# Kernel tuning notes

Hardware: AMD Instinct MI355X
Metric: run time of the kernel (lower is better)

## Reference

```python
import jax, jax.numpy as jnp
import numpy as np

N, E, C, H = 100000, 3200000, 4, 64
EPS = 1e-8


def setup_inputs() -> dict:
    key = jax.random.key(0)
    k1, k2, k3, k4, k5, k6, k7 = jax.random.split(key, 7)
    x = jax.random.uniform(k1, (N, C), dtype=jnp.float32)            # [pm10, u10, v10, aux]
    pos = jax.random.normal(k2, (N, 2), dtype=jnp.float32)           # node coordinates
    edge_index = jax.random.randint(k3, (2, E), 0, N, dtype=jnp.int64)
    # PhysicsFluxLayer edge MLP: in = [x_i, x_j, wind_proj, dist] -> hidden
    fan_in = 2 * C + 2
    mlp_w = jax.random.normal(k4, (H, fan_in), dtype=jnp.float32) / np.sqrt(fan_in)
    mlp_b = jnp.zeros((H,), dtype=jnp.float32)
    # output head (module inits to zero; use small random values for a non-degenerate baseline)
    head_w = jax.random.normal(k5, (1, H), dtype=jnp.float32) * 0.02
    head_b = jax.random.normal(k6, (1,), dtype=jnp.float32) * 0.02
    return {"x": x, "pos": pos, "mlp_w": mlp_w, "mlp_b": mlp_b,
            "head_w": head_w, "head_b": head_b, "edge_index": edge_index}


def reference(x, pos, mlp_w, mlp_b, head_w, head_b, edge_index):
    src = edge_index[0]   # j (message source)
    dst = edge_index[1]   # i (message target)
    u10, v10 = x[:, 1], x[:, 2]
    # edge geometry: direction i -> j and distance
    d = pos[src] - pos[dst]                                  # [E,2]
    dist = jnp.sqrt(jnp.sum(d * d, axis=1) + EPS)            # [E]
    dhat = d / dist[:, None]
    # source wind projected onto the edge direction (advective transport term)
    wind_proj = u10[src] * dhat[:, 0] + v10[src] * dhat[:, 1]  # [E]
    edge_feat = jnp.concatenate(
        [x[dst], x[src], wind_proj[:, None], dist[:, None]], axis=1)  # [E, 2C+2]
    msg = jax.nn.relu(edge_feat @ mlp_w.T + mlp_b)            # [E,H]
    flux = jax.ops.segment_sum(msg, dst, num_segments=N)      # [N,H] scatter-add
    delta_pm10 = flux @ head_w.T + head_b                     # [N,1]
    pm10_next = jax.nn.softplus(x[:, 0:1] + delta_pm10)       # [N,1]
    return pm10_next, delta_pm10
```

## Files before the change

### kernel.cpp

```cpp
#include <hip/hip_runtime.h>
#include <hip/hip_bf16.h>


#define HID    64
#define EPSV   1e-8f
#define BNODES 256
#define CAP    10240
#define MAXB   512
#define BLK_SC 512
#define RPT_SC 25
#define LSTAGE (BLK_SC * RPT_SC)
#define BLK_C  256
#define SLOTW  20
#define OVF_CAP 65536

typedef _Float16 half8 __attribute__((ext_vector_type(8)));
typedef _Float16 half2_t __attribute__((ext_vector_type(2)));
typedef float f32x4 __attribute__((ext_vector_type(4)));

__device__ __forceinline__ unsigned int packh2(float a, float b) {
    union { half2_t h; unsigned int u; } v;
    v.h = half2_t{(_Float16)a, (_Float16)b};
    return v.u;
}

__device__ __forceinline__ void feat_from_rows(float4 xs, float4 ps4,
                                               float4 xd, float4 pd4,
                                               float* f) {
    float d0 = ps4.x - pd4.x;
    float d1 = ps4.y - pd4.y;
    float dist = sqrtf(fmaf(d0, d0, fmaf(d1, d1, EPSV)));
    float inv = 1.0f / dist;
    float wind = (xs.y * d0 + xs.z * d1) * inv;
    f[0] = xd.x; f[1] = xd.y; f[2] = xd.z; f[3] = xd.w;
    f[4] = xs.x; f[5] = xs.y; f[6] = xs.z; f[7] = xs.w;
    f[8] = wind; f[9] = dist;
}

__device__ __forceinline__ float mlp_scalar_g(const float* __restrict__ mlp_w,
                                              const float* __restrict__ mlp_b,
                                              const float* __restrict__ head_w,
                                              const float* f) {
    float sacc = 0.0f;
    for (int h = 0; h < HID; h++) {
        const float* wr = mlp_w + h * 10;
        float a = mlp_b[h];
        a = fmaf(wr[0], f[0], a); a = fmaf(wr[1], f[1], a);
        a = fmaf(wr[2], f[2], a); a = fmaf(wr[3], f[3], a);
        a = fmaf(wr[4], f[4], a); a = fmaf(wr[5], f[5], a);
        a = fmaf(wr[6], f[6], a); a = fmaf(wr[7], f[7], a);
        a = fmaf(wr[8], f[8], a); a = fmaf(wr[9], f[9], a);
        a = fmaxf(a, 0.0f);
        sacc = fmaf(head_w[h], a, sacc);
    }
    return sacc;
}

__global__ __launch_bounds__(512) void prep_kernel(
    const float4* __restrict__ x, const float2* __restrict__ pos,
    float4* __restrict__ xpos, float* __restrict__ delta_extra,
    unsigned long long* g_ptr64, int* ovf_cnt, int N, int PB)
{
    int n = blockIdx.x * 512 + threadIdx.x;
    if (n < N) {
        float4 xr = x[n];
        float2 pr = pos[n];
        xpos[2 * n]     = xr;
        xpos[2 * n + 1] = make_float4(pr.x, pr.y, 0.0f, 0.0f);
        delta_extra[n] = 0.0f;
    }
    if (n < PB) g_ptr64[n] = 0ull;
    if (n == 0) *ovf_cnt = 0;
}

__global__ __launch_bounds__(BLK_SC) void scatter_kernel(
    const int* __restrict__ srcs, const int* __restrict__ dsts,
    int E, int B,
    unsigned long long* g_ptr64, unsigned int* __restrict__ sorted,
    int2* __restrict__ ovf, int* ovf_cnt)
{
    __shared__ int hist[MAXB];
    __shared__ int base[MAXB];
    __shared__ int run[MAXB];
    __shared__ int wsum[BLK_SC / 64];
    __shared__ unsigned int lstage[LSTAGE];

    int tid  = threadIdx.x;
    int lane = tid & 63;
    int wid  = tid >> 6;
    int lo = blockIdx.x * (BLK_SC * RPT_SC);

    int es[RPT_SC], ed[RPT_SC];
    bool ev[RPT_SC];
    #pragma unroll
    for (int r = 0; r < RPT_SC; r++) {
        int e = lo + r * BLK_SC + tid;
        bool okr = (e < E);
        ev[r] = okr;
        int ee = okr ? e : 0;
        es[r] = srcs[ee];
        ed[r] = dsts[ee];
    }

    for (int b2 = tid; b2 < MAXB; b2 += BLK_SC) { hist[b2] = 0; run[b2] = 0; }
    __syncthreads();
    #pragma unroll
    for (int r = 0; r < RPT_SC; r++)
        if (ev[r]) atomicAdd(&hist[ed[r] >> 8], 1);
    __syncthreads();

    int PB = (B + 1) >> 1;
    for (int p = tid; p < PB; p += BLK_SC) {
        int b0 = 2 * p, b1 = 2 * p + 1;
        unsigned long long h0 = (unsigned int)hist[b0];
        unsigned long long h1 = (b1 < B) ? (unsigned int)hist[b1] : 0ull;
        unsigned long long comb = h0 | (h1 << 32);
        unsigned long long old = 0ull;
        if (comb) old = atomicAdd(&g_ptr64[p], comb);
        base[b0] = (int)(old & 0xffffffffull);
        if (b1 < B) base[b1] = (int)(old >> 32);
    }
    int v = hist[tid];
    int x = v;
    #pragma unroll
    for (int m = 1; m < 64; m <<= 1) {
        int y = __shfl_up(x, m, 64);
        if (lane >= m) x += y;
    }
    if (lane == 63) wsum[wid] = x;
    __syncthreads();
    if (tid == 0) {
        int a = 0;
        #pragma unroll
        for (int j = 0; j < BLK_SC / 64; j++) { int t = wsum[j]; wsum[j] = a; a += t; }
    }
    __syncthreads();
    hist[tid] = wsum[wid] + x - v;
    __syncthreads();

    #pragma unroll
    for (int r = 0; r < RPT_SC; r++) {
        if (ev[r]) {
            int d = ed[r];
            int b = d >> 8;
            int rk = atomicAdd(&run[b], 1);
            lstage[hist[b] + rk] =
                ((unsigned int)es[r] << 8) | (unsigned int)(d & 255);
        }
    }
    __syncthreads();

    for (int b = wid; b < B; b += BLK_SC / 64) {
        int cnt = run[b];
        int gb  = base[b];
        int lp  = hist[b];
        for (int t = lane; t < cnt; t += 64) {
            unsigned int pay = lstage[lp + t];
            int rel = gb + t;
            if (rel < CAP) {
                sorted[(size_t)b * CAP + rel] = pay;
            } else {
                int o = atomicAdd(ovf_cnt, 1);
                if (o < OVF_CAP)
                    ovf[o] = make_int2((int)(pay >> 8), (b << 8) | (int)(pay & 255u));
            }
        }
    }
}

__global__ __launch_bounds__(BLK_C, 4) void compute_kernel(
    const float4* __restrict__ xpos,
    const float* __restrict__ mlp_w, const float* __restrict__ mlp_b,
    const float* __restrict__ head_w,
    const unsigned int* __restrict__ sorted,
    const unsigned long long* __restrict__ g_ptr64,
    float* __restrict__ partial, int BB, int ksh)
{
    __shared__ __align__(16) unsigned int stage[4 * 64 * SLOTW];
    __shared__ float acc[BNODES];
    int tid  = threadIdx.x;
    int wave = tid >> 6;
    int lane = tid & 63;
    int col  = lane & 15;
    int quad = lane >> 4;
    int wbase = wave * 64 * SLOTW;

    acc[tid] = 0.0f;

    {
        unsigned int* slotp = &stage[wbase + lane * SLOTW];
        slotp[5] = 0u;
        *(uint2*)(slotp + 6) = make_uint2(0u, 0u);
        *(uint4*)(slotp + 8) = make_uint4(0u, 0u, 0u, 0u);
        *(uint4*)(slotp + 12) = make_uint4(0u, 0u, 0u, 0u);
    }

    half8 wfr[4];
    f32x4 bias4[4], hw4[4];
    #pragma unroll
    for (int c = 0; c < 4; c++) {
        int h = c * 16 + col;
        half8 wf = half8{0, 0, 0, 0, 0, 0, 0, 0};
        if (quad == 0) {
            #pragma unroll
            for (int j = 0; j < 8; j++) wf[j] = (_Float16)mlp_w[h * 10 + j];
        } else if (quad == 1) {
            wf[0] = (_Float16)mlp_w[h * 10 + 8];
            wf[1] = (_Float16)mlp_w[h * 10 + 9];
        }
        wfr[c] = wf;
        bias4[c] = *(const f32x4*)&mlp_b[c * 16 + quad * 4];
        hw4[c]   = *(const f32x4*)&head_w[c * 16 + quad * 4];
    }
    __syncthreads();

    int b    = blockIdx.x >> ksh;
    int part = blockIdx.x & ((1 << ksh) - 1);
    unsigned long long gp = g_ptr64[b >> 1];
    int cnt = (b & 1) ? (int)(gp >> 32) : (int)(gp & 0xffffffffull);
    cnt = min(cnt, CAP);
    int e0 = (cnt * part) >> ksh;
    int e1 = (cnt * (part + 1)) >> ksh;
    const unsigned int* sp = sorted + (size_t)b * CAP;
    int nbase = b << 8;

    int i = e0 + tid;
    bool ok = (i < e1);
    unsigned int pay = (e0 < e1) ? sp[ok ? i : e0] : 0u;
    int s  = (int)(pay >> 8);
    int dl = (int)(pay & 255u);
    float4 xs  = xpos[2 * s];
    float4 ps4 = xpos[2 * s + 1];
    float4 xd  = xpos[2 * (nbase + dl)];
    float4 pd4 = xpos[2 * (nbase + dl) + 1];

    for (int i0 = e0; i0 < e1; i0 += BLK_C) {
        bool cok = ok;
        int  cdl = dl;
        float f[10];
        feat_from_rows(xs, ps4, xd, pd4, f);
        unsigned int pk0 = packh2(f[0], f[1]);
        unsigned int pk1 = packh2(f[2], f[3]);
        unsigned int pk2 = packh2(f[4], f[5]);
        unsigned int pk3 = packh2(f[6], f[7]);
        unsigned int pk4 = packh2(f[8], f[9]);

        int ni = i0 + BLK_C + tid;
        ok = (ni < e1);
        pay = sp[ok ? ni : e0];
        s  = (int)(pay >> 8);
        dl = (int)(pay & 255u);
        xs  = xpos[2 * s];
        ps4 = xpos[2 * s + 1];
        xd  = xpos[2 * (nbase + dl)];
        pd4 = xpos[2 * (nbase + dl) + 1];

        unsigned int* slotp = &stage[wbase + lane * SLOTW];
        *(uint4*)slotp = make_uint4(pk0, pk1, pk2, pk3);
        slotp[4] = pk4;

        float mysum = 0.0f;
        #pragma unroll
        for (int eg = 0; eg < 4; eg++) {
            const half8 fb = *(const half8*)&stage[wbase + (eg * 16 + col) * SLOTW + quad * 4];
            float sacc = 0.0f;
            #pragma unroll
            for (int c = 0; c < 4; c++) {
                f32x4 d = __builtin_amdgcn_mfma_f32_16x16x32_f16(wfr[c], fb, bias4[c], 0, 0, 0);
                sacc = fmaf(hw4[c][0], fmaxf(d[0], 0.f), sacc);
                sacc = fmaf(hw4[c][1], fmaxf(d[1], 0.f), sacc);
                sacc = fmaf(hw4[c][2], fmaxf(d[2], 0.f), sacc);
                sacc = fmaf(hw4[c][3], fmaxf(d[3], 0.f), sacc);
            }
            sacc += __shfl_xor(sacc, 16, 64);
            sacc += __shfl_xor(sacc, 32, 64);
            if (quad == eg) mysum = sacc;
        }
        if (cok) atomicAdd(&acc[cdl], mysum);
    }
    __syncthreads();
    partial[(size_t)part * BB + nbase + tid] = acc[tid];
}

__global__ __launch_bounds__(256) void ovf_kernel(
    const float4* __restrict__ x, const float2* __restrict__ pos,
    const float* __restrict__ mlp_w, const float* __restrict__ mlp_b,
    const float* __restrict__ head_w,
    const int2* __restrict__ ovf, const int* __restrict__ ovf_cnt,
    float* __restrict__ delta_extra)
{
    int cnt = min(*ovf_cnt, OVF_CAP);
    for (int i = blockIdx.x * blockDim.x + threadIdx.x; i < cnt;
         i += gridDim.x * blockDim.x) {
        int2 sd = ovf[i];
        float4 xs = x[sd.x], xd = x[sd.y];
        float2 ps = pos[sd.x], pd = pos[sd.y];
        float f[10];
        feat_from_rows(xs, make_float4(ps.x, ps.y, 0, 0),
                       xd, make_float4(pd.x, pd.y, 0, 0), f);
        unsafeAtomicAdd(&delta_extra[sd.y], mlp_scalar_g(mlp_w, mlp_b, head_w, f));
    }
}

__global__ __launch_bounds__(512) void final_kernel(
    const float* __restrict__ xf,
    const float* __restrict__ partial, int BB,
    const float* __restrict__ delta_extra,
    const float* __restrict__ head_b,
    float* __restrict__ out, int N, int kpart)
{
    int n = blockIdx.x * 512 + threadIdx.x;
    if (n >= N) return;
    float delta = delta_extra[n] + head_b[0];
    for (int p = 0; p < kpart; p++)
        delta += partial[(size_t)p * BB + n];
    float v = xf[4 * n] + delta;
    float sp = fmaxf(v, 0.0f) + log1pf(expf(-fabsf(v)));
    out[n] = sp;
    out[N + n] = delta;
}

__global__ __launch_bounds__(256) void edge_kernel_fallback(
    const float4* __restrict__ x, const float2* __restrict__ pos,
    const float* __restrict__ mlp_w, const float* __restrict__ mlp_b,
    const float* __restrict__ head_w,
    const int* __restrict__ srcs, const int* __restrict__ dsts,
    float* __restrict__ delta_acc, int E)
{
    long e = (long)blockIdx.x * 256 + threadIdx.x;
    if (e >= E) return;
    int s = srcs[e], d = dsts[e];
    float4 xs = x[s], xd = x[d];
    float2 ps = pos[s], pd = pos[d];
    float f[10];
    feat_from_rows(xs, make_float4(ps.x, ps.y, 0, 0),
                   xd, make_float4(pd.x, pd.y, 0, 0), f);
    unsafeAtomicAdd(&delta_acc[d], mlp_scalar_g(mlp_w, mlp_b, head_w, f));
}

__global__ __launch_bounds__(256) void node_kernel_fallback(
    const float* __restrict__ xf, const float* __restrict__ delta_acc,
    const float* __restrict__ head_b, float* __restrict__ out, int N)
{
    int n = blockIdx.x * 256 + threadIdx.x;
    if (n >= N) return;
    float delta = delta_acc[n] + head_b[0];
    float v = xf[4 * n] + delta;
    float sp = fmaxf(v, 0.0f) + log1pf(expf(-fabsf(v)));
    out[n] = sp;
    out[N + n] = delta;
}

static inline size_t align_up(size_t v, size_t a) { return (v + a - 1) & ~(a - 1); }

extern "C" void kernel_launch(void* const* d_in, const int* in_sizes, int n_in,
                              void* d_out, int out_size, void* d_ws, size_t ws_size,
                              hipStream_t stream) {
    const float4* x      = (const float4*)d_in[0];
    const float2* pos    = (const float2*)d_in[1];
    const float*  mlp_w  = (const float*)d_in[2];
    const float*  mlp_b  = (const float*)d_in[3];
    const float*  head_w = (const float*)d_in[4];
    const float*  head_b = (const float*)d_in[5];
    const int*    ei     = (const int*)d_in[6];

    int N = in_sizes[0] / 4;
    int E = in_sizes[6] / 2;
    const int* srcs = ei;
    const int* dsts = ei + E;
    int B  = (N + BNODES - 1) / BNODES;
    int PB = (B + 1) >> 1;
    int BB = B * BNODES;

    size_t off = 0;
    float* delta_extra = (float*)((char*)d_ws + off);
    off = align_up(off + (size_t)N * 4, 256);
    float4* xpos = (float4*)((char*)d_ws + off);
    off = align_up(off + (size_t)N * 32, 256);
    unsigned long long* g_ptr64 = (unsigned long long*)((char*)d_ws + off);
    off = align_up(off + (size_t)PB * 8, 256);
    int* ovf_cnt = (int*)((char*)d_ws + off);
    off = align_up(off + 64, 256);
    int2* ovf = (int2*)((char*)d_ws + off);
    off = align_up(off + (size_t)OVF_CAP * 8, 256);
    unsigned int* sorted = (unsigned int*)((char*)d_ws + off);
    off = align_up(off + (size_t)B * CAP * 4, 256);
    float* partial = (float*)((char*)d_ws + off);

    int kpart = 8, ksh = 3;
    if (off + (size_t)8 * BB * 4 > ws_size) { kpart = 4; ksh = 2; }
    size_t off_end = off + (size_t)kpart * BB * 4;
    bool fast = (off_end <= ws_size) && (B <= MAXB);

    if (fast) {
        int pgrid = (N + 511) / 512;
        prep_kernel<<<pgrid, 512, 0, stream>>>(x, pos, xpos, delta_extra,
                                               g_ptr64, ovf_cnt, N, PB);
        int sgrid = (E + LSTAGE - 1) / LSTAGE;
        scatter_kernel<<<sgrid, BLK_SC, 0, stream>>>(srcs, dsts, E, B,
                                                     g_ptr64, sorted, ovf, ovf_cnt);
        compute_kernel<<<B << ksh, BLK_C, 0, stream>>>(xpos, mlp_w, mlp_b, head_w,
                                                       sorted, g_ptr64, partial, BB, ksh);
        ovf_kernel<<<16, 256, 0, stream>>>(x, pos, mlp_w, mlp_b, head_w,
                                           ovf, ovf_cnt, delta_extra);
        final_kernel<<<(N + 511) / 512, 512, 0, stream>>>(
            (const float*)x, partial, BB, delta_extra, head_b, (float*)d_out, N, kpart);
    } else {
        float* delta = (float*)d_ws;
        hipMemsetAsync(delta, 0, (size_t)N * sizeof(float), stream);
        edge_kernel_fallback<<<(int)((E + 255) / 256), 256, 0, stream>>>(
            x, pos, mlp_w, mlp_b, head_w, srcs, dsts, delta, E);
        node_kernel_fallback<<<(N + 255) / 256, 256, 0, stream>>>(
            (const float*)x, delta, head_b, (float*)d_out, N);
    }
}
```

Before: 157.1 us.

## Fuse prep and overflow kernels, cache dst rows in LDS, deepen prefetch

The prep kernel is replaced by a memset plus node-row packing and fp16 weight-fragment building inside the scatter kernel. The overflow kernel is folded into the compute kernel's part-0 blocks. The scatter now ranks edges once with a single atomic pass and writes through a precomputed destination table instead of a second local atomic pass. The compute kernel stages its 256 destination rows in LDS, loads prebuilt weight fragments, and uses a three-stage software prefetch rotation. The goal is fewer launches and less gather and atomic work, at the cost of more LDS in the scatter kernel (two 12800-entry arrays), which may lower its occupancy.

```diff
diff --git a/kernel.cpp b/kernel.cpp
--- a/kernel.cpp
+++ b/kernel.cpp
@@ -56,39 +56,26 @@
     return sacc;
 }
 
-__global__ __launch_bounds__(512) void prep_kernel(
-    const float4* __restrict__ x, const float2* __restrict__ pos,
-    float4* __restrict__ xpos, float* __restrict__ delta_extra,
-    unsigned long long* g_ptr64, int* ovf_cnt, int N, int PB)
-{
-    int n = blockIdx.x * 512 + threadIdx.x;
-    if (n < N) {
-        float4 xr = x[n];
-        float2 pr = pos[n];
-        xpos[2 * n]     = xr;
-        xpos[2 * n + 1] = make_float4(pr.x, pr.y, 0.0f, 0.0f);
-        delta_extra[n] = 0.0f;
-    }
-    if (n < PB) g_ptr64[n] = 0ull;
-    if (n == 0) *ovf_cnt = 0;
-}
-
 __global__ __launch_bounds__(BLK_SC) void scatter_kernel(
     const int* __restrict__ srcs, const int* __restrict__ dsts,
-    int E, int B,
+    int E, int B, int N,
+    const float4* __restrict__ x, const float2* __restrict__ pos,
+    const float* __restrict__ mlp_w,
+    float4* __restrict__ xpos, uint4* __restrict__ wbuf,
     unsigned long long* g_ptr64, unsigned int* __restrict__ sorted,
     int2* __restrict__ ovf, int* ovf_cnt)
 {
     __shared__ int hist[MAXB];
     __shared__ int base[MAXB];
-    __shared__ int run[MAXB];
+    __shared__ int pfx[MAXB];
     __shared__ int wsum[BLK_SC / 64];
-    __shared__ unsigned int lstage[LSTAGE];
+    __shared__ unsigned int lpay[LSTAGE];
+    __shared__ unsigned int ldst[LSTAGE];
 
     int tid  = threadIdx.x;
     int lane = tid & 63;
     int wid  = tid >> 6;
-    int lo = blockIdx.x * (BLK_SC * RPT_SC);
+    int lo = blockIdx.x * LSTAGE;
 
     int es[RPT_SC], ed[RPT_SC];
     bool ev[RPT_SC];
@@ -102,11 +89,48 @@
         ed[r] = dsts[ee];
     }
 
-    for (int b2 = tid; b2 < MAXB; b2 += BLK_SC) { hist[b2] = 0; run[b2] = 0; }
-    __syncthreads();
+    for (int b2 = tid; b2 < MAXB; b2 += BLK_SC) hist[b2] = 0;
+
+    {
+        int nper = (N + gridDim.x - 1) / gridDim.x;
+        int n0 = blockIdx.x * nper;
+        int n1 = min(n0 + nper, N);
+        for (int n = n0 + tid; n < n1; n += BLK_SC) {
+            float4 xr = x[n];
+            float2 pr = pos[n];
+            xpos[2 * n]     = xr;
+            xpos[2 * n + 1] = make_float4(pr.x, pr.y, 0.0f, 0.0f);
+        }
+    }
+    if (blockIdx.x == 0 && tid < 64) {
+        int colw = tid & 15, quadw = tid >> 4;
+        #pragma unroll
+        for (int c = 0; c < 4; c++) {
+            int h = c * 16 + colw;
+            half8 wf = half8{0, 0, 0, 0, 0, 0, 0, 0};
+            if (quadw == 0) {
+                #pragma unroll
+                for (int j = 0; j < 8; j++) wf[j] = (_Float16)mlp_w[h * 10 + j];
+            } else if (quadw == 1) {
+                wf[0] = (_Float16)mlp_w[h * 10 + 8];
+                wf[1] = (_Float16)mlp_w[h * 10 + 9];
+            }
+            union { half8 h8; uint4 u4; } cv;
+            cv.h8 = wf;
+            wbuf[c * 64 + tid] = cv.u4;
+        }
+    }
+    __syncthreads();
+
     #pragma unroll
-    for (int r = 0; r < RPT_SC; r++)
-        if (ev[r]) atomicAdd(&hist[ed[r] >> 8], 1);
+    for (int r = 0; r < RPT_SC; r++) {
+        if (ev[r]) {
+            int b = ed[r] >> 8;
+            int rk = atomicAdd(&hist[b], 1);
+            es[r] = (es[r] << 8) | (ed[r] & 255);
+            ed[r] = (b << 14) | rk;
+        }
+    }
     __syncthreads();
 
     int PB = (B + 1) >> 1;
@@ -121,13 +145,13 @@
         if (b1 < B) base[b1] = (int)(old >> 32);
     }
     int v = hist[tid];
-    int x = v;
+    int xs_ = v;
     #pragma unroll
     for (int m = 1; m < 64; m <<= 1) {
-        int y = __shfl_up(x, m, 64);
-        if (lane >= m) x += y;
-    }
-    if (lane == 63) wsum[wid] = x;
+        int y = __shfl_up(xs_, m, 64);
+        if (lane >= m) xs_ += y;
+    }
+    if (lane == 63) wsum[wid] = xs_;
     __syncthreads();
     if (tid == 0) {
         int a = 0;
@@ -135,48 +159,49 @@
         for (int j = 0; j < BLK_SC / 64; j++) { int t = wsum[j]; wsum[j] = a; a += t; }
     }
     __syncthreads();
-    hist[tid] = wsum[wid] + x - v;
+    pfx[tid] = wsum[wid] + xs_ - v;
     __syncthreads();
 
     #pragma unroll
     for (int r = 0; r < RPT_SC; r++) {
         if (ev[r]) {
-            int d = ed[r];
-            int b = d >> 8;
-            int rk = atomicAdd(&run[b], 1);
-            lstage[hist[b] + rk] =
-                ((unsigned int)es[r] << 8) | (unsigned int)(d & 255);
-        }
-    }
-    __syncthreads();
-
-    for (int b = wid; b < B; b += BLK_SC / 64) {
-        int cnt = run[b];
-        int gb  = base[b];
-        int lp  = hist[b];
-        for (int t = lane; t < cnt; t += 64) {
-            unsigned int pay = lstage[lp + t];
-            int rel = gb + t;
+            int b  = ed[r] >> 14;
+            int rk = ed[r] & 0x3FFF;
+            int p  = pfx[b] + rk;
+            unsigned int pay = (unsigned int)es[r];
+            lpay[p] = pay;
+            int rel = base[b] + rk;
             if (rel < CAP) {
-                sorted[(size_t)b * CAP + rel] = pay;
+                ldst[p] = (unsigned int)b * CAP + (unsigned int)rel;
             } else {
+                ldst[p] = 0xFFFFFFFFu;
                 int o = atomicAdd(ovf_cnt, 1);
                 if (o < OVF_CAP)
                     ovf[o] = make_int2((int)(pay >> 8), (b << 8) | (int)(pay & 255u));
             }
         }
     }
+    __syncthreads();
+
+    int cnt_blk = min(E - lo, LSTAGE);
+    for (int t = tid; t < cnt_blk; t += BLK_SC) {
+        unsigned int d = ldst[t];
+        if (d != 0xFFFFFFFFu) sorted[d] = lpay[t];
+    }
 }
 
 __global__ __launch_bounds__(BLK_C, 4) void compute_kernel(
     const float4* __restrict__ xpos,
+    const uint4* __restrict__ wbuf,
     const float* __restrict__ mlp_w, const float* __restrict__ mlp_b,
     const float* __restrict__ head_w,
     const unsigned int* __restrict__ sorted,
     const unsigned long long* __restrict__ g_ptr64,
-    float* __restrict__ partial, int BB, int ksh)
+    const int2* __restrict__ ovf, const int* __restrict__ ovf_cnt,
+    float* __restrict__ partial, int BB, int ksh, int N)
 {
     __shared__ __align__(16) unsigned int stage[4 * 64 * SLOTW];
+    __shared__ __align__(16) float4 drows[2 * BNODES];
     __shared__ float acc[BNODES];
     int tid  = threadIdx.x;
     int wave = tid >> 6;
@@ -185,7 +210,17 @@
     int quad = lane >> 4;
     int wbase = wave * 64 * SLOTW;
 
+    int b    = blockIdx.x >> ksh;
+    int part = blockIdx.x & ((1 << ksh) - 1);
+    int nbase = b << 8;
+
     acc[tid] = 0.0f;
+
+    {
+        int lim = 2 * N - 1;
+        drows[tid]       = xpos[min(2 * nbase + tid, lim)];
+        drows[tid + 256] = xpos[min(2 * nbase + tid + 256, lim)];
+    }
 
     {
         unsigned int* slotp = &stage[wbase + lane * SLOTW];
@@ -199,119 +234,110 @@
     f32x4 bias4[4], hw4[4];
     #pragma unroll
     for (int c = 0; c < 4; c++) {
-        int h = c * 16 + col;
-        half8 wf = half8{0, 0, 0, 0, 0, 0, 0, 0};
-        if (quad == 0) {
-            #pragma unroll
-            for (int j = 0; j < 8; j++) wf[j] = (_Float16)mlp_w[h * 10 + j];
-        } else if (quad == 1) {
-            wf[0] = (_Float16)mlp_w[h * 10 + 8];
-            wf[1] = (_Float16)mlp_w[h * 10 + 9];
-        }
-        wfr[c] = wf;
+        union { uint4 u4; half8 h8; } cv;
+        cv.u4 = wbuf[c * 64 + lane];
+        wfr[c] = cv.h8;
         bias4[c] = *(const f32x4*)&mlp_b[c * 16 + quad * 4];
         hw4[c]   = *(const f32x4*)&head_w[c * 16 + quad * 4];
     }
     __syncthreads();
 
-    int b    = blockIdx.x >> ksh;
-    int part = blockIdx.x & ((1 << ksh) - 1);
     unsigned long long gp = g_ptr64[b >> 1];
     int cnt = (b & 1) ? (int)(gp >> 32) : (int)(gp & 0xffffffffull);
     cnt = min(cnt, CAP);
     int e0 = (cnt * part) >> ksh;
     int e1 = (cnt * (part + 1)) >> ksh;
     const unsigned int* sp = sorted + (size_t)b * CAP;
-    int nbase = b << 8;
-
-    int i = e0 + tid;
-    bool ok = (i < e1);
-    unsigned int pay = (e0 < e1) ? sp[ok ? i : e0] : 0u;
-    int s  = (int)(pay >> 8);
-    int dl = (int)(pay & 255u);
-    float4 xs  = xpos[2 * s];
-    float4 ps4 = xpos[2 * s + 1];
-    float4 xd  = xpos[2 * (nbase + dl)];
-    float4 pd4 = xpos[2 * (nbase + dl) + 1];
-
-    for (int i0 = e0; i0 < e1; i0 += BLK_C) {
-        bool cok = ok;
-        int  cdl = dl;
-        float f[10];
-        feat_from_rows(xs, ps4, xd, pd4, f);
-        unsigned int pk0 = packh2(f[0], f[1]);
-        unsigned int pk1 = packh2(f[2], f[3]);
-        unsigned int pk2 = packh2(f[4], f[5]);
-        unsigned int pk3 = packh2(f[6], f[7]);
-        unsigned int pk4 = packh2(f[8], f[9]);
-
-        int ni = i0 + BLK_C + tid;
-        ok = (ni < e1);
-        pay = sp[ok ? ni : e0];
-        s  = (int)(pay >> 8);
-        dl = (int)(pay & 255u);
-        xs  = xpos[2 * s];
-        ps4 = xpos[2 * s + 1];
-        xd  = xpos[2 * (nbase + dl)];
-        pd4 = xpos[2 * (nbase + dl) + 1];
-
-        unsigned int* slotp = &stage[wbase + lane * SLOTW];
-        *(uint4*)slotp = make_uint4(pk0, pk1, pk2, pk3);
-        slotp[4] = pk4;
-
-        float mysum = 0.0f;
-        #pragma unroll
-        for (int eg = 0; eg < 4; eg++) {
-            const half8 fb = *(const half8*)&stage[wbase + (eg * 16 + col) * SLOTW + quad * 4];
-            float sacc = 0.0f;
+
+    if (e0 < e1) {
+        unsigned int p0, p1, p2;
+        float4 xA, pA, xB, pB, xC, pC;
+        {
+            int i = e0 + tid;
+            p0 = sp[(i < e1) ? i : e0];
+            int i1 = i + BLK_C;
+            p1 = sp[(i1 < e1) ? i1 : e0];
+            int s0 = (int)(p0 >> 8);
+            xA = xpos[2 * s0];
+            pA = xpos[2 * s0 + 1];
+        }
+
+        auto body = [&](int i0, unsigned int pc, unsigned int pn,
+                        unsigned int& pn2, float4 xc, float4 psc,
+                        float4& xn, float4& psn) {
+            bool cok = (i0 + tid) < e1;
+            int dl = (int)(pc & 255u);
+            int i2 = i0 + 2 * BLK_C + tid;
+            pn2 = sp[(i2 < e1) ? i2 : e0];
+            int sn = (int)(pn >> 8);
+            xn  = xpos[2 * sn];
+            psn = xpos[2 * sn + 1];
+            float4 xd  = drows[2 * dl];
+            float4 pd4 = drows[2 * dl + 1];
+            float f[10];
+            feat_from_rows(xc, psc, xd, pd4, f);
+            unsigned int* slotp = &stage[wbase + lane * SLOTW];
+            *(uint4*)slotp = make_uint4(packh2(f[0], f[1]), packh2(f[2], f[3]),
+                                        packh2(f[4], f[5]), packh2(f[6], f[7]));
+            slotp[4] = packh2(f[8], f[9]);
+
+            float mysum = 0.0f;
             #pragma unroll
-            for (int c = 0; c < 4; c++) {
-                f32x4 d = __builtin_amdgcn_mfma_f32_16x16x32_f16(wfr[c], fb, bias4[c], 0, 0, 0);
-                sacc = fmaf(hw4[c][0], fmaxf(d[0], 0.f), sacc);
-                sacc = fmaf(hw4[c][1], fmaxf(d[1], 0.f), sacc);
-                sacc = fmaf(hw4[c][2], fmaxf(d[2], 0.f), sacc);
-                sacc = fmaf(hw4[c][3], fmaxf(d[3], 0.f), sacc);
+            for (int eg = 0; eg < 4; eg++) {
+                const half8 fb = *(const half8*)&stage[wbase + (eg * 16 + col) * SLOTW + quad * 4];
+                float sacc = 0.0f;
+                #pragma unroll
+                for (int c = 0; c < 4; c++) {
+                    f32x4 d = __builtin_amdgcn_mfma_f32_16x16x32_f16(wfr[c], fb, bias4[c], 0, 0, 0);
+                    sacc = fmaf(hw4[c][0], fmaxf(d[0], 0.f), sacc);
+                    sacc = fmaf(hw4[c][1], fmaxf(d[1], 0.f), sacc);
+                    sacc = fmaf(hw4[c][2], fmaxf(d[2], 0.f), sacc);
+                    sacc = fmaf(hw4[c][3], fmaxf(d[3], 0.f), sacc);
+                }
+                sacc += __shfl_xor(sacc, 16, 64);
+                sacc += __shfl_xor(sacc, 32, 64);
+                if (quad == eg) mysum = sacc;
             }
-            sacc += __shfl_xor(sacc, 16, 64);
-            sacc += __shfl_xor(sacc, 32, 64);
-            if (quad == eg) mysum = sacc;
-        }
-        if (cok) atomicAdd(&acc[cdl], mysum);
+            if (cok) atomicAdd(&acc[dl], mysum);
+        };
+
+        int i0 = e0;
+        for (;;) {
+            body(i0, p0, p1, p2, xA, pA, xB, pB);
+            i0 += BLK_C; if (i0 >= e1) break;
+            body(i0, p1, p2, p0, xB, pB, xC, pC);
+            i0 += BLK_C; if (i0 >= e1) break;
+            body(i0, p2, p0, p1, xC, pC, xA, pA);
+            i0 += BLK_C; if (i0 >= e1) break;
+        }
     }
     __syncthreads();
     partial[(size_t)part * BB + nbase + tid] = acc[tid];
-}
-
-__global__ __launch_bounds__(256) void ovf_kernel(
-    const float4* __restrict__ x, const float2* __restrict__ pos,
-    const float* __restrict__ mlp_w, const float* __restrict__ mlp_b,
-    const float* __restrict__ head_w,
-    const int2* __restrict__ ovf, const int* __restrict__ ovf_cnt,
-    float* __restrict__ delta_extra)
-{
-    int cnt = min(*ovf_cnt, OVF_CAP);
-    for (int i = blockIdx.x * blockDim.x + threadIdx.x; i < cnt;
-         i += gridDim.x * blockDim.x) {
-        int2 sd = ovf[i];
-        float4 xs = x[sd.x], xd = x[sd.y];
-        float2 ps = pos[sd.x], pd = pos[sd.y];
-        float f[10];
-        feat_from_rows(xs, make_float4(ps.x, ps.y, 0, 0),
-                       xd, make_float4(pd.x, pd.y, 0, 0), f);
-        unsafeAtomicAdd(&delta_extra[sd.y], mlp_scalar_g(mlp_w, mlp_b, head_w, f));
+
+    if (part == 0) {
+        __syncthreads();
+        int oc = min(*ovf_cnt, OVF_CAP);
+        for (int idx = tid; idx < oc; idx += BLK_C) {
+            int2 sd = ovf[idx];
+            if ((sd.y >> 8) == b) {
+                float f[10];
+                feat_from_rows(xpos[2 * sd.x], xpos[2 * sd.x + 1],
+                               xpos[2 * sd.y], xpos[2 * sd.y + 1], f);
+                unsafeAtomicAdd(&partial[sd.y], mlp_scalar_g(mlp_w, mlp_b, head_w, f));
+            }
+        }
     }
 }
 
 __global__ __launch_bounds__(512) void final_kernel(
     const float* __restrict__ xf,
     const float* __restrict__ partial, int BB,
-    const float* __restrict__ delta_extra,
     const float* __restrict__ head_b,
     float* __restrict__ out, int N, int kpart)
 {
     int n = blockIdx.x * 512 + threadIdx.x;
     if (n >= N) return;
-    float delta = delta_extra[n] + head_b[0];
+    float delta = head_b[0];
     for (int p = 0; p < kpart; p++)
         delta += partial[(size_t)p * BB + n];
     float v = xf[4 * n] + delta;
@@ -373,14 +399,15 @@
     int BB = B * BNODES;
 
     size_t off = 0;
-    float* delta_extra = (float*)((char*)d_ws + off);
-    off = align_up(off + (size_t)N * 4, 256);
+    unsigned long long* g_ptr64 = (unsigned long long*)((char*)d_ws + off);
+    off = align_up(off + (size_t)PB * 8, 64);
+    int* ovf_cnt = (int*)((char*)d_ws + off);
+    size_t zero_bytes = off + 64;
+    off = align_up(off + 64, 256);
     float4* xpos = (float4*)((char*)d_ws + off);
     off = align_up(off + (size_t)N * 32, 256);
-    unsigned long long* g_ptr64 = (unsigned long long*)((char*)d_ws + off);
-    off = align_up(off + (size_t)PB * 8, 256);
-    int* ovf_cnt = (int*)((char*)d_ws + off);
-    off = align_up(off + 64, 256);
+    uint4* wbuf = (uint4*)((char*)d_ws + off);
+    off = align_up(off + (size_t)4 * 64 * 16, 256);
     int2* ovf = (int2*)((char*)d_ws + off);
     off = align_up(off + (size_t)OVF_CAP * 8, 256);
     unsigned int* sorted = (unsigned int*)((char*)d_ws + off);
@@ -393,18 +420,16 @@
     bool fast = (off_end <= ws_size) && (B <= MAXB);
 
     if (fast) {
-        int pgrid = (N + 511) / 512;
-        prep_kernel<<<pgrid, 512, 0, stream>>>(x, pos, xpos, delta_extra,
-                                               g_ptr64, ovf_cnt, N, PB);
+        hipMemsetAsync(d_ws, 0, zero_bytes, stream);
         int sgrid = (E + LSTAGE - 1) / LSTAGE;
-        scatter_kernel<<<sgrid, BLK_SC, 0, stream>>>(srcs, dsts, E, B,
-                                                     g_ptr64, sorted, ovf, ovf_cnt);
-        compute_kernel<<<B << ksh, BLK_C, 0, stream>>>(xpos, mlp_w, mlp_b, head_w,
-                                                       sorted, g_ptr64, partial, BB, ksh);
-        ovf_kernel<<<16, 256, 0, stream>>>(x, pos, mlp_w, mlp_b, head_w,
-                                           ovf, ovf_cnt, delta_extra);
+        scatter_kernel<<<sgrid, BLK_SC, 0, stream>>>(
+            srcs, dsts, E, B, N, x, pos, mlp_w,
+            xpos, wbuf, g_ptr64, sorted, ovf, ovf_cnt);
+        compute_kernel<<<B << ksh, BLK_C, 0, stream>>>(
+            xpos, wbuf, mlp_w, mlp_b, head_w, sorted, g_ptr64,
+            ovf, ovf_cnt, partial, BB, ksh, N);
         final_kernel<<<(N + 511) / 512, 512, 0, stream>>>(
-            (const float*)x, partial, BB, delta_extra, head_b, (float*)d_out, N, kpart);
+            (const float*)x, partial, BB, head_b, (float*)d_out, N, kpart);
     } else {
         float* delta = (float*)d_ws;
         hipMemsetAsync(delta, 0, (size_t)N * sizeof(float), stream);
```

Result: faster. 144.4 us (-8.1%).
